# Performance work log

Measured on AMD Instinct MI355X. Metric: run time of the kernel, lower is better.

## Reference

```python
import jax, jax.numpy as jnp
import numpy as np

N_ATOMS = 200000
MAX_DEG = 6
DEG_COUNTS = [2000, 40000, 60000, 58000, 38000, 1500, 500]  # atoms of degree 0..6, sorted by degree
_OFF = np.concatenate([[0], np.cumsum(DEG_COUNTS)])
BATCH = 1024
N_TASKS = 12
NAF = 75
BN_SCALE = np.float32(1.0 / np.sqrt(1.0 + 1e-5))  # eval-mode BN, running stats (0, 1)


def _split(x):
    # static degree slicing (atoms sorted by degree)
    return [x[_OFF[d]:_OFF[d + 1]] for d in range(MAX_DEG + 1)]


def graph_conv(x, adjs, W, b):
    # W: [2*MAX_DEG+1, in, out]; per degree d>=1 weights (2(d-1): neighbors, 2d-1: self), last: degree-0 self
    sp = _split(x)
    outs = [None] * (MAX_DEG + 1)
    for d in range(1, MAX_DEG + 1):
        summed = x[adjs[d - 1]].sum(axis=1)  # [n_d, in] sum over d neighbors
        o = summed @ W[2 * (d - 1)] + b[2 * (d - 1)]
        o = o + sp[d] @ W[2 * d - 1] + b[2 * d - 1]
        outs[d] = o
    outs[0] = sp[0] @ W[2 * MAX_DEG] + b[2 * MAX_DEG]
    return jax.nn.relu(jnp.concatenate(outs, axis=0))


def graph_pool(x, adjs):
    # max over {self} U neighbors, per degree
    sp = _split(x)
    outs = [sp[0]]
    for d in range(1, MAX_DEG + 1):
        neigh = x[adjs[d - 1]]  # [n_d, d, nf]
        outs.append(jnp.concatenate([sp[d][:, None, :], neigh], axis=1).max(axis=1))
    return jnp.concatenate(outs, axis=0)


def bn(x, gamma, beta):
    return x * (gamma * BN_SCALE) + beta


def _forward(atom_features, conv0_W, conv0_b, conv1_W, conv1_b,
             bn0_gamma, bn0_beta, bn1_gamma, bn1_beta, bn2_gamma, bn2_beta,
             bn3_gamma, bn3_beta, dense0_W, dense0_b, dense1_W, dense1_b,
             reg_W, reg_b, unc_W, unc_b, membership, adjs, n_samples):
    x = graph_conv(atom_features, adjs, conv0_W, conv0_b)
    x = bn(x, bn0_gamma, bn0_beta)
    x = graph_pool(x, adjs)
    x = graph_conv(x, adjs, conv1_W, conv1_b)
    x = bn(x, bn1_gamma, bn1_beta)
    x = graph_pool(x, adjs)
    x = bn(jax.nn.relu(x @ dense0_W + dense0_b), bn2_gamma, bn2_beta)
    x = bn(jax.nn.relu(x @ dense1_W + dense1_b), bn3_gamma, bn3_beta)
    fp = jnp.tanh(jax.ops.segment_sum(x, membership, num_segments=BATCH))  # GraphGather
    out = (fp @ reg_W + reg_b)[:n_samples]
    log_var = (fp @ unc_W + unc_b)[:n_samples]
    var = jnp.exp(log_var)
    return (out, var, out, log_var, fp)


def setup_inputs():
    key = jax.random.key(0)
    ks = jax.random.split(key, 32)
    inp = {}
    inp['atom_features'] = jax.random.normal(ks[0], (N_ATOMS, NAF), jnp.float32)
    inp['degree_slice'] = jnp.stack([jnp.asarray(_OFF[:-1], jnp.int32), jnp.asarray(DEG_COUNTS, jnp.int32)], axis=1)
    inp['membership'] = jax.random.randint(ks[1], (N_ATOMS,), 0, BATCH, jnp.int32)
    inp['n_samples'] = BATCH
    for d in range(1, MAX_DEG + 1):
        inp['deg_adj_%d' % d] = jax.random.randint(ks[1 + d], (DEG_COUNTS[d], d), 0, N_ATOMS, jnp.int32)
    def w(k, shape):
        return jax.random.normal(k, shape, jnp.float32) * 0.05
    nW = 2 * MAX_DEG + 1
    inp['conv0_W'] = w(ks[8], (nW, NAF, 128)); inp['conv0_b'] = w(ks[9], (nW, 128))
    inp['conv1_W'] = w(ks[10], (nW, 128, 128)); inp['conv1_b'] = w(ks[11], (nW, 128))
    inp['bn0_gamma'] = 1.0 + w(ks[12], (128,)); inp['bn0_beta'] = w(ks[13], (128,))
    inp['bn1_gamma'] = 1.0 + w(ks[14], (128,)); inp['bn1_beta'] = w(ks[15], (128,))
    inp['bn2_gamma'] = 1.0 + w(ks[16], (64,)); inp['bn2_beta'] = w(ks[17], (64,))
    inp['bn3_gamma'] = 1.0 + w(ks[18], (64,)); inp['bn3_beta'] = w(ks[19], (64,))
    inp['dense0_W'] = w(ks[20], (128, 64)); inp['dense0_b'] = w(ks[21], (64,))
    inp['dense1_W'] = w(ks[22], (64, 64)); inp['dense1_b'] = w(ks[23], (64,))
    inp['reg_W'] = w(ks[24], (64, N_TASKS)); inp['reg_b'] = w(ks[25], (N_TASKS,))
    inp['unc_W'] = w(ks[26], (64, N_TASKS)); inp['unc_b'] = w(ks[27], (N_TASKS,))
    return inp


def reference(atom_features, conv0_W, conv0_b, conv1_W, conv1_b,
              bn0_gamma, bn0_beta, bn1_gamma, bn1_beta, bn2_gamma, bn2_beta,
              bn3_gamma, bn3_beta, dense0_W, dense0_b, dense1_W, dense1_b,
              reg_W, reg_b, unc_W, unc_b,
              degree_slice, membership, n_samples,
              deg_adj_1, deg_adj_2, deg_adj_3, deg_adj_4, deg_adj_5, deg_adj_6):
    adjs = [deg_adj_1, deg_adj_2, deg_adj_3, deg_adj_4, deg_adj_5, deg_adj_6]
    return _forward(atom_features, conv0_W, conv0_b, conv1_W, conv1_b,
                    bn0_gamma, bn0_beta, bn1_gamma, bn1_beta, bn2_gamma, bn2_beta,
                    bn3_gamma, bn3_beta, dense0_W, dense0_b, dense1_W, dense1_b,
                    reg_W, reg_b, unc_W, unc_b, membership, adjs, n_samples)
```

## Files before the change

### kernel.cpp

```cpp
#include <hip/hip_runtime.h>
#include <math.h>

constexpr int OFFS[8] = {0, 2000, 42000, 102000, 160000, 198000, 199500, 200000};
constexpr int CNT[7]  = {2000, 40000, 60000, 58000, 38000, 1500, 500};
constexpr int C_OFF[8] = {0, 32, 657, 1595, 2502, 3096, 3120, 3128};
constexpr int P_OFF[8] = {0, 250, 5250, 12750, 20000, 24750, 24938, 25001};
#define BN_SCALE_C 0.9999950000374997f

struct Adjs { const int* a[6]; };

typedef __attribute__((ext_vector_type(8))) short bf16x8;
typedef __attribute__((ext_vector_type(4))) float f32x4;

__device__ __forceinline__ void split1(float x, ushort& h, ushort& l) {
    const unsigned u = __float_as_uint(x);
    h = (ushort)(u >> 16);
    const float r = x - __uint_as_float(u & 0xffff0000u);
    l = (ushort)(__float_as_uint(r) >> 16);
}

__global__ __launch_bounds__(256)
void w1_convert_kernel(const float* __restrict__ W, ushort* __restrict__ hi,
                       ushort* __restrict__ lo) {
    const int t = blockIdx.x * 256 + threadIdx.x;
    if (t >= 13 * 8 * 4 * 64 * 8) return;
    const int i = t & 7, l = (t >> 3) & 63, ks = (t >> 9) & 3,
              g = (t >> 11) & 7, s = t >> 14;
    const int col = g * 16 + (l & 15);
    const int k = ks * 32 + (l >> 4) * 8 + i;
    ushort h, lw;
    split1(W[(size_t)(s * 128 + k) * 128 + col], h, lw);
    hi[t] = h; lo[t] = lw;
}

__global__ __launch_bounds__(256)
void w0_convert_kernel(const float* __restrict__ W, ushort* __restrict__ hi,
                       ushort* __restrict__ lo) {
    const int t = blockIdx.x * 256 + threadIdx.x;
    if (t >= 7 * 8 * 5 * 64 * 8) return;
    const int i = t & 7;
    const int r = t >> 3;
    const int l = r & 63;
    const int r2 = r >> 6;
    const int ks = r2 % 5;
    const int r3 = r2 / 5;
    const int g = r3 & 7, d = r3 >> 3;
    const int col = g * 16 + (l & 15);
    const int k = ks * 32 + (l >> 4) * 8 + i;
    float v = 0.f;
    if (d == 0) {
        if (k < 75) v = W[(size_t)(12 * 75 + k) * 128 + col];
    } else {
        if (k < 75)       v = W[(size_t)((2 * d - 2) * 75 + k) * 128 + col];
        else if (k < 150) v = W[(size_t)((2 * d - 1) * 75 + (k - 75)) * 128 + col];
    }
    ushort h, lw;
    split1(v, h, lw);
    hi[t] = h; lo[t] = lw;
}

template<int KSTEPS, int SROW>
__device__ __forceinline__ void mfma_gemm(const ushort* sa_hi, const ushort* sa_lo,
                                          const ushort* wp_hi, const ushort* wp_lo,
                                          f32x4 acc[8], int l, int w)
{
    const int lr = l & 15, lq = l >> 4;
    const size_t lb = (size_t)l * 8;
    #pragma unroll
    for (int ks = 0; ks < KSTEPS; ++ks) {
        const int kb = ks * 32 + lq * 8;
        const bf16x8 ah = *(const bf16x8*)(sa_hi + (size_t)(w * 16 + lr) * SROW + kb);
        const bf16x8 al = *(const bf16x8*)(sa_lo + (size_t)(w * 16 + lr) * SROW + kb);
        bf16x8 bh0 = *(const bf16x8*)(wp_hi + (size_t)(0 * KSTEPS + ks) * 512 + lb);
        bf16x8 bl0 = *(const bf16x8*)(wp_lo + (size_t)(0 * KSTEPS + ks) * 512 + lb);
        bf16x8 bh1 = *(const bf16x8*)(wp_hi + (size_t)(1 * KSTEPS + ks) * 512 + lb);
        bf16x8 bl1 = *(const bf16x8*)(wp_lo + (size_t)(1 * KSTEPS + ks) * 512 + lb);
        #pragma unroll
        for (int g = 0; g < 8; ++g) {
            bf16x8 bh2 = bh0, bl2 = bl0;
            if (g < 6) {
                bh2 = *(const bf16x8*)(wp_hi + (size_t)((g + 2) * KSTEPS + ks) * 512 + lb);
                bl2 = *(const bf16x8*)(wp_lo + (size_t)((g + 2) * KSTEPS + ks) * 512 + lb);
            }
            acc[g] = __builtin_amdgcn_mfma_f32_16x16x32_bf16(ah, bh0, acc[g], 0, 0, 0);
            acc[g] = __builtin_amdgcn_mfma_f32_16x16x32_bf16(al, bh0, acc[g], 0, 0, 0);
            acc[g] = __builtin_amdgcn_mfma_f32_16x16x32_bf16(ah, bl0, acc[g], 0, 0, 0);
            bh0 = bh1; bl0 = bl1; bh1 = bh2; bl1 = bl2;
        }
    }
}

__device__ __forceinline__ void mfma_epilogue(f32x4 acc[8], float* fs,
                                              const float* s_eb, float* out,
                                              int a0, int nat, int tid)
{
    const int l = tid & 63, w = tid >> 6, lr = l & 15, lq = l >> 4;
    __syncthreads();
    #pragma unroll
    for (int g = 0; g < 8; ++g)
        #pragma unroll
        for (int r = 0; r < 4; ++r)
            fs[(size_t)(w * 16 + lq * 4 + r) * 132 + g * 16 + lr] = acc[g][r];
    __syncthreads();
    #pragma unroll
    for (int p = 0; p < 8; ++p) {
        const int row = p * 8 + (tid >> 5);
        if (row < nat) {
            const int c = (tid & 31) * 4;
            const float4 v  = *(const float4*)&fs[(size_t)row * 132 + c];
            const float4 bb = *(const float4*)&s_eb[c];
            const float4 gs = *(const float4*)&s_eb[128 + c];
            const float4 be = *(const float4*)&s_eb[256 + c];
            float4 o;
            o.x = fmaxf(v.x + bb.x, 0.f) * gs.x + be.x;
            o.y = fmaxf(v.y + bb.y, 0.f) * gs.y + be.y;
            o.z = fmaxf(v.z + bb.z, 0.f) * gs.z + be.z;
            o.w = fmaxf(v.w + bb.w, 0.f) * gs.w + be.w;
            *(float4*)(out + (size_t)(a0 + row) * 128 + c) = o;
        }
    }
}

template<int D>
__device__ __forceinline__ void conv0_body(int tile, const float* __restrict__ x,
    const ushort* __restrict__ wp_hi, const ushort* __restrict__ wp_lo,
    const float* __restrict__ b, const float* __restrict__ gamma,
    const float* __restrict__ beta, const int* __restrict__ adjp,
    float* __restrict__ out, ushort* s_ahi, ushort* s_alo, int* s_adj,
    float* s_eb, int tid)
{
    constexpr int SROW = 168;
    const int a0 = OFFS[D] + tile * 64;
    const int nat = min(64, OFFS[D + 1] - a0);

    if (tid < 128) {
        float bb;
        if constexpr (D > 0)
            bb = b[(2 * D - 2) * 128 + tid] + b[(2 * D - 1) * 128 + tid];
        else
            bb = b[12 * 128 + tid];
        s_eb[tid] = bb;
        s_eb[128 + tid] = gamma[tid] * BN_SCALE_C;
        s_eb[256 + tid] = beta[tid];
    }
    if constexpr (D > 0) {
        for (int e = tid; e < 64 * D; e += 256) {
            const int al = e / D;
            if (al < nat)
                s_adj[e] = adjp[(size_t)(a0 - OFFS[D] + al) * D + (e - al * D)];
        }
        __syncthreads();
    }
    if constexpr (D == 0) {
        for (int e = tid; e < 64 * 85; e += 256) {
            const int al = e / 85, k = 75 + e - (e / 85) * 85;
            s_ahi[al * SROW + k] = 0; s_alo[al * SROW + k] = 0;
        }
    } else {
        for (int e = tid; e < 64 * 10; e += 256) {
            const int al = e / 10, k = 150 + e - (e / 10) * 10;
            s_ahi[al * SROW + k] = 0; s_alo[al * SROW + k] = 0;
        }
    }
    #pragma unroll 4
    for (int p = 0; p < 19; ++p) {
        const int e = p * 256 + tid;
        if (e < 4800) {
            const int al = e / 75;
            const int kk = e - al * 75;
            if (al < nat) {
                const float self = x[(size_t)(a0 + al) * 75 + kk];
                ushort h, l;
                if constexpr (D > 0) {
                    float sum = 0.f;
                    #pragma unroll
                    for (int i = 0; i < D; ++i)
                        sum += x[(size_t)s_adj[al * D + i] * 75 + kk];
                    split1(sum, h, l);
                    s_ahi[al * SROW + kk] = h; s_alo[al * SROW + kk] = l;
                    split1(self, h, l);
                    s_ahi[al * SROW + 75 + kk] = h; s_alo[al * SROW + 75 + kk] = l;
                } else {
                    split1(self, h, l);
                    s_ahi[al * SROW + kk] = h; s_alo[al * SROW + kk] = l;
                }
            }
        }
    }
    __syncthreads();

    const int l = tid & 63, w = tid >> 6;
    f32x4 acc[8];
    #pragma unroll
    for (int g = 0; g < 8; ++g) acc[g] = (f32x4){0.f, 0.f, 0.f, 0.f};
    mfma_gemm<5, SROW>(s_ahi, s_alo, wp_hi + (size_t)D * 20480,
                       wp_lo + (size_t)D * 20480, acc, l, w);
    mfma_epilogue(acc, (float*)s_ahi, s_eb, out, a0, nat, tid);
}

__global__ __launch_bounds__(256, 3)
void conv0_merged(const float* __restrict__ x, const ushort* __restrict__ wp_hi,
                  const ushort* __restrict__ wp_lo, const float* __restrict__ b,
                  const float* __restrict__ gamma, const float* __restrict__ beta,
                  Adjs adj, float* __restrict__ out)
{
    __shared__ ushort s_a[2][64 * 168];
    __shared__ int s_adj[64 * 6];
    __shared__ float s_eb[384];
    const int blk = blockIdx.x, tid = threadIdx.x;
    #define C0(D) conv0_body<D>(blk - C_OFF[D], x, wp_hi, wp_lo, b, gamma, beta, \
        (D > 0) ? adj.a[D - 1] : nullptr, out, s_a[0], s_a[1], s_adj, s_eb, tid)
    if      (blk < C_OFF[1]) C0(0);
    else if (blk < C_OFF[2]) C0(1);
    else if (blk < C_OFF[3]) C0(2);
    else if (blk < C_OFF[4]) C0(3);
    else if (blk < C_OFF[5]) C0(4);
    else if (blk < C_OFF[6]) C0(5);
    else                     C0(6);
    #undef C0
}

template<int D, bool PHASE0>
__device__ __forceinline__ void conv1_stage(const float* __restrict__ x,
    ushort* s_ahi, ushort* s_alo, const int* s_adj, int a0, int nat, int tid)
{
    constexpr int SROW = 136;
    #pragma unroll 2
    for (int p = 0; p < 8; ++p) {
        const int e = p * 256 + tid;
        const int al = e >> 5, c = e & 31;
        if (al < nat) {
            float4 v;
            if (PHASE0 && D > 0) {
                v = make_float4(0.f, 0.f, 0.f, 0.f);
                #pragma unroll
                for (int i = 0; i < D; ++i) {
                    const float4 t = *((const float4*)(x + (size_t)s_adj[al * D + i] * 128) + c);
                    v.x += t.x; v.y += t.y; v.z += t.z; v.w += t.w;
                }
            } else {
                v = *((const float4*)(x + (size_t)(a0 + al) * 128) + c);
            }
            ushort4 h, lo;
            split1(v.x, h.x, lo.x); split1(v.y, h.y, lo.y);
            split1(v.z, h.z, lo.z); split1(v.w, h.w, lo.w);
            *(ushort4*)&s_ahi[al * SROW + c * 4] = h;
            *(ushort4*)&s_alo[al * SROW + c * 4] = lo;
        }
    }
}

template<int D>
__device__ __forceinline__ void conv1_body(int tile, const float* __restrict__ x,
    const ushort* __restrict__ wp_hi, const ushort* __restrict__ wp_lo,
    const float* __restrict__ b, const float* __restrict__ gamma,
    const float* __restrict__ beta, const int* __restrict__ adjp,
    float* __restrict__ out, ushort* s_ahi, ushort* s_alo, int* s_adj,
    float* s_eb, int tid)
{
    constexpr int SROW = 136;
    const int a0 = OFFS[D] + tile * 64;
    const int nat = min(64, OFFS[D + 1] - a0);

    if (tid < 128) {
        float bb;
        if constexpr (D > 0)
            bb = b[(2 * D - 2) * 128 + tid] + b[(2 * D - 1) * 128 + tid];
        else
            bb = b[12 * 128 + tid];
        s_eb[tid] = bb;
        s_eb[128 + tid] = gamma[tid] * BN_SCALE_C;
        s_eb[256 + tid] = beta[tid];
    }
    if constexpr (D > 0) {
        for (int e = tid; e < 64 * D; e += 256) {
            const int al = e / D;
            if (al < nat)
                s_adj[e] = adjp[(size_t)(a0 - OFFS[D] + al) * D + (e - al * D)];
        }
        __syncthreads();
    }

    const int l = tid & 63, w = tid >> 6;
    f32x4 acc[8];
    #pragma unroll
    for (int g = 0; g < 8; ++g) acc[g] = (f32x4){0.f, 0.f, 0.f, 0.f};

    conv1_stage<D, true>(x, s_ahi, s_alo, s_adj, a0, nat, tid);
    __syncthreads();
    {
        const size_t wb = (size_t)((D == 0) ? 12 : (2 * D - 2)) * 16384;
        mfma_gemm<4, SROW>(s_ahi, s_alo, wp_hi + wb, wp_lo + wb, acc, l, w);
    }
    if constexpr (D > 0) {
        __syncthreads();
        conv1_stage<D, false>(x, s_ahi, s_alo, s_adj, a0, nat, tid);
        __syncthreads();
        const size_t wb = (size_t)(2 * D - 1) * 16384;
        mfma_gemm<4, SROW>(s_ahi, s_alo, wp_hi + wb, wp_lo + wb, acc, l, w);
    }
    mfma_epilogue(acc, (float*)s_ahi, s_eb, out, a0, nat, tid);
}

__global__ __launch_bounds__(256, 4)
void conv1_merged(const float* __restrict__ x, const ushort* __restrict__ wp_hi,
                  const ushort* __restrict__ wp_lo, const float* __restrict__ b,
                  const float* __restrict__ gamma, const float* __restrict__ beta,
                  Adjs adj, float* __restrict__ out)
{
    __shared__ ushort s_a[2][64 * 136];
    __shared__ int s_adj[64 * 6];
    __shared__ float s_eb[384];
    const int blk = blockIdx.x, tid = threadIdx.x;
    #define C1(D) conv1_body<D>(blk - C_OFF[D], x, wp_hi, wp_lo, b, gamma, beta, \
        (D > 0) ? adj.a[D - 1] : nullptr, out, s_a[0], s_a[1], s_adj, s_eb, tid)
    if      (blk < C_OFF[1]) C1(0);
    else if (blk < C_OFF[2]) C1(1);
    else if (blk < C_OFF[3]) C1(2);
    else if (blk < C_OFF[4]) C1(3);
    else if (blk < C_OFF[5]) C1(4);
    else if (blk < C_OFF[6]) C1(5);
    else                     C1(6);
    #undef C1
}

template<int D>
__device__ __forceinline__ void pool_body(int tile, const float* __restrict__ x,
    const int* __restrict__ adjp, float* __restrict__ out, int tid)
{
    const int tx = tid & 31;
    const int ai = tile * 8 + (tid >> 5);
    if (ai >= CNT[D]) return;
    const int a = OFFS[D] + ai;
    float4 v = *((const float4*)(x + (size_t)a * 128) + tx);
    if constexpr (D > 0) {
        #pragma unroll
        for (int i = 0; i < D; ++i) {
            const int n = adjp[(size_t)ai * D + i];
            const float4 t = *((const float4*)(x + (size_t)n * 128) + tx);
            v.x = fmaxf(v.x, t.x); v.y = fmaxf(v.y, t.y);
            v.z = fmaxf(v.z, t.z); v.w = fmaxf(v.w, t.w);
        }
    }
    *((float4*)(out + (size_t)a * 128) + tx) = v;
}

__global__ __launch_bounds__(256)
void pool_merged(const float* __restrict__ x, Adjs adj, float* __restrict__ out)
{
    const int blk = blockIdx.x, tid = threadIdx.x;
    #define PB(D) pool_body<D>(blk - P_OFF[D], x, (D > 0) ? adj.a[D - 1] : nullptr, out, tid)
    if      (blk < P_OFF[1]) PB(0);
    else if (blk < P_OFF[2]) PB(1);
    else if (blk < P_OFF[3]) PB(2);
    else if (blk < P_OFF[4]) PB(3);
    else if (blk < P_OFF[5]) PB(4);
    else if (blk < P_OFF[6]) PB(5);
    else                     PB(6);
    #undef PB
}

template<int D>
__device__ __forceinline__ void d0_body(int tile, const float* __restrict__ x,
    const float* __restrict__ W, const float* __restrict__ b,
    const float* __restrict__ gamma, const float* __restrict__ beta,
    const int* __restrict__ adjp, float* __restrict__ out,
    float* s_a , int* s_adj, int tid)
{
    const int a0 = OFFS[D] + tile * 64;
    const int nat = min(64, OFFS[D + 1] - a0);

    if constexpr (D > 0) {
        for (int e = tid; e < 64 * D; e += 256) {
            const int al = e / D;
            if (al < nat)
                s_adj[e] = adjp[(size_t)(a0 - OFFS[D] + al) * D + (e - al * D)];
        }
        __syncthreads();
    }
    {
        const int tx4 = tid & 31, ag = tid >> 5;
        #pragma unroll
        for (int ap = 0; ap < 8; ++ap) {
            const int al = ap * 8 + ag;
            if (al < nat) {
                float4 v = *((const float4*)(x + (size_t)(a0 + al) * 128) + tx4);
                if constexpr (D > 0) {
                    #pragma unroll
                    for (int i = 0; i < D; ++i) {
                        const float4 t =
                            *((const float4*)(x + (size_t)s_adj[al * D + i] * 128) + tx4);
                        v.x = fmaxf(v.x, t.x); v.y = fmaxf(v.y, t.y);
                        v.z = fmaxf(v.z, t.z); v.w = fmaxf(v.w, t.w);
                    }
                }
                *(float4*)&s_a[al * 132 + tx4 * 4] = v;
            }
        }
    }
    __syncthreads();

    const int tx = tid & 15, ty = tid >> 4;
    float acc[4][4];
    #pragma unroll
    for (int i = 0; i < 4; ++i)
        #pragma unroll
        for (int j = 0; j < 4; ++j) acc[i][j] = 0.f;

    #pragma unroll 4
    for (int k4 = 0; k4 < 32; ++k4) {
        float4 wk[4];
        #pragma unroll
        for (int kk = 0; kk < 4; ++kk)
            wk[kk] = *(const float4*)(W + (size_t)(k4 * 4 + kk) * 64 + tx * 4);
        #pragma unroll
        for (int i = 0; i < 4; ++i) {
            const float4 av = *(const float4*)&s_a[(ty * 4 + i) * 132 + k4 * 4];
            acc[i][0] = fmaf(av.x, wk[0].x, acc[i][0]);
            acc[i][1] = fmaf(av.x, wk[0].y, acc[i][1]);
            acc[i][2] = fmaf(av.x, wk[0].z, acc[i][2]);
            acc[i][3] = fmaf(av.x, wk[0].w, acc[i][3]);
            acc[i][0] = fmaf(av.y, wk[1].x, acc[i][0]);
            acc[i][1] = fmaf(av.y, wk[1].y, acc[i][1]);
            acc[i][2] = fmaf(av.y, wk[1].z, acc[i][2]);
            acc[i][3] = fmaf(av.y, wk[1].w, acc[i][3]);
            acc[i][0] = fmaf(av.z, wk[2].x, acc[i][0]);
            acc[i][1] = fmaf(av.z, wk[2].y, acc[i][1]);
            acc[i][2] = fmaf(av.z, wk[2].z, acc[i][2]);
            acc[i][3] = fmaf(av.z, wk[2].w, acc[i][3]);
            acc[i][0] = fmaf(av.w, wk[3].x, acc[i][0]);
            acc[i][1] = fmaf(av.w, wk[3].y, acc[i][1]);
            acc[i][2] = fmaf(av.w, wk[3].z, acc[i][2]);
            acc[i][3] = fmaf(av.w, wk[3].w, acc[i][3]);
        }
    }
    const int j = tx * 4;
    float bb[4], gs[4], be[4];
    #pragma unroll
    for (int c = 0; c < 4; ++c) {
        bb[c] = b[j + c]; gs[c] = gamma[j + c] * BN_SCALE_C; be[c] = beta[j + c];
    }
    #pragma unroll
    for (int i = 0; i < 4; ++i) {
        const int al = ty * 4 + i;
        if (al < nat) {
            float4 o;
            o.x = fmaxf(acc[i][0] + bb[0], 0.f) * gs[0] + be[0];
            o.y = fmaxf(acc[i][1] + bb[1], 0.f) * gs[1] + be[1];
            o.z = fmaxf(acc[i][2] + bb[2], 0.f) * gs[2] + be[2];
            o.w = fmaxf(acc[i][3] + bb[3], 0.f) * gs[3] + be[3];
            *(float4*)(out + (size_t)(a0 + al) * 64 + j) = o;
        }
    }
}

__global__ __launch_bounds__(256, 4)
void dense0_pool_merged(const float* __restrict__ x, const float* __restrict__ W,
                        const float* __restrict__ b, const float* __restrict__ gamma,
                        const float* __restrict__ beta, Adjs adj,
                        float* __restrict__ out)
{
    __shared__ float s_a[64 * 132];
    __shared__ int s_adj[64 * 6];
    const int blk = blockIdx.x, tid = threadIdx.x;
    #define D0(D) d0_body<D>(blk - C_OFF[D], x, W, b, gamma, beta, \
        (D > 0) ? adj.a[D - 1] : nullptr, out, s_a, s_adj, tid)
    if      (blk < C_OFF[1]) D0(0);
    else if (blk < C_OFF[2]) D0(1);
    else if (blk < C_OFF[3]) D0(2);
    else if (blk < C_OFF[4]) D0(3);
    else if (blk < C_OFF[5]) D0(4);
    else if (blk < C_OFF[6]) D0(5);
    else                     D0(6);
    #undef D0
}

__global__ void zero_counts_kernel(int* __restrict__ counts) {
    counts[blockIdx.x * 256 + threadIdx.x] = 0;
}

__global__ __launch_bounds__(256)
void hist_kernel(const int* __restrict__ mem, int* __restrict__ counts) {
    const int a = blockIdx.x * 256 + threadIdx.x;
    if (a < 200000) atomicAdd(&counts[mem[a]], 1);
}

__global__ __launch_bounds__(1024)
void scan_kernel(const int* __restrict__ counts, int* __restrict__ starts,
                 int* __restrict__ cursor) {
    __shared__ int s[1024];
    const int tid = threadIdx.x;
    s[tid] = counts[tid];
    __syncthreads();
    #pragma unroll
    for (int off = 1; off < 1024; off <<= 1) {
        const int v = (tid >= off) ? s[tid - off] : 0;
        __syncthreads();
        s[tid] += v;
        __syncthreads();
    }
    const int st = (tid == 0) ? 0 : s[tid - 1];
    starts[tid] = st;
    cursor[tid] = st;
    if (tid == 1023) starts[1024] = s[1023];
}

__global__ __launch_bounds__(256)
void scatter_kernel(const int* __restrict__ mem, int* __restrict__ cursor,
                    int* __restrict__ idx) {
    const int a = blockIdx.x * 256 + threadIdx.x;
    if (a < 200000) {
        const int p = atomicAdd(&cursor[mem[a]], 1);
        idx[p] = a;
    }
}

__global__ __launch_bounds__(256, 4)
void seg_dense1_kernel(const float* __restrict__ y0, const float* __restrict__ W,
                       const float* __restrict__ b, const float* __restrict__ gamma,
                       const float* __restrict__ beta, const int* __restrict__ idx,
                       const int* __restrict__ starts, float* __restrict__ accum)
{
    __shared__ float s_a[64][68];
    __shared__ float s_w[64][64];
    __shared__ float s_red[16][64];
    const int tid = threadIdx.x;
    const int seg = blockIdx.x;
    const int s0 = starts[seg];
    const int cnt = starts[seg + 1] - s0;

    #pragma unroll
    for (int p = 0; p < 4; ++p) {
        const int f = p * 256 + tid;
        const int r = f >> 4, c = (f & 15) * 4;
        *(float4*)&s_w[r][c] = *(const float4*)(W + r * 64 + c);
    }

    const int tx = tid & 15, ty = tid >> 4;
    const int j = tx * 4;
    float bb[4], gs[4], be[4];
    #pragma unroll
    for (int c = 0; c < 4; ++c) {
        bb[c] = b[j + c]; gs[c] = gamma[j + c] * BN_SCALE_C; be[c] = beta[j + c];
    }
    float facc[4] = {0.f, 0.f, 0.f, 0.f};

    for (int t0 = 0; t0 < cnt; t0 += 64) {
        const int nt = min(64, cnt - t0);
        __syncthreads();
        #pragma unroll
        for (int p = 0; p < 4; ++p) {
            const int e = p * 256 + tid;
            const int al = e >> 4, c = e & 15;
            if (al < nt) {
                const int a = idx[s0 + t0 + al];
                *(float4*)&s_a[al][c * 4] = *((const float4*)(y0 + (size_t)a * 64) + c);
            }
        }
        __syncthreads();
        float acc[4][4];
        #pragma unroll
        for (int i = 0; i < 4; ++i)
            #pragma unroll
            for (int c = 0; c < 4; ++c) acc[i][c] = 0.f;
        #pragma unroll 8
        for (int k = 0; k < 64; ++k) {
            const float4 w = *(float4*)&s_w[k][tx * 4];
            #pragma unroll
            for (int i = 0; i < 4; ++i) {
                const float av = s_a[ty * 4 + i][k];
                acc[i][0] = fmaf(av, w.x, acc[i][0]);
                acc[i][1] = fmaf(av, w.y, acc[i][1]);
                acc[i][2] = fmaf(av, w.z, acc[i][2]);
                acc[i][3] = fmaf(av, w.w, acc[i][3]);
            }
        }
        #pragma unroll
        for (int i = 0; i < 4; ++i) {
            if (ty * 4 + i < nt) {
                #pragma unroll
                for (int c = 0; c < 4; ++c)
                    facc[c] += fmaxf(acc[i][c] + bb[c], 0.f) * gs[c] + be[c];
            }
        }
    }
    __syncthreads();
    #pragma unroll
    for (int c = 0; c < 4; ++c) s_red[ty][j + c] = facc[c];
    __syncthreads();
    if (tid < 64) {
        float s = 0.f;
        #pragma unroll
        for (int q = 0; q < 16; ++q) s += s_red[q][tid];
        accum[(size_t)seg * 64 + tid] = s;
    }
}

__global__ __launch_bounds__(256)
void final_kernel(const float* __restrict__ accum,
                  const float* __restrict__ regW, const float* __restrict__ regb,
                  const float* __restrict__ uncW, const float* __restrict__ uncb,
                  float* __restrict__ out)
{
    __shared__ float s_f[256];
    const int tid = threadIdx.x;
    const int rl = tid >> 6;
    const int c = tid & 63;
    const int r = blockIdx.x * 4 + rl;
    const float f = tanhf(accum[(size_t)r * 64 + c]);
    out[49152 + (size_t)r * 64 + c] = f;
    s_f[tid] = f;
    __syncthreads();
    if (c < 24) {
        const bool isreg = (c < 12);
        const int t = isreg ? c : c - 12;
        const float* Wm = isreg ? regW : uncW;
        float a = isreg ? regb[t] : uncb[t];
        #pragma unroll 8
        for (int k = 0; k < 64; ++k)
            a = fmaf(s_f[rl * 64 + k], Wm[k * 12 + t], a);
        if (isreg) {
            out[(size_t)r * 12 + t] = a;
            out[24576 + (size_t)r * 12 + t] = a;
        } else {
            out[36864 + (size_t)r * 12 + t] = a;
            out[12288 + (size_t)r * 12 + t] = expf(a);
        }
    }
}

extern "C" void kernel_launch(void* const* d_in, const int* in_sizes, int n_in,
                              void* d_out, int out_size, void* d_ws, size_t ws_size,
                              hipStream_t stream)
{
    const float* atom_features = (const float*)d_in[0];
    const int*   membership    = (const int*)d_in[2];
    Adjs adj;
    for (int d = 1; d <= 6; ++d) adj.a[d - 1] = (const int*)d_in[3 + d];
    const float* conv0_W = (const float*)d_in[10];
    const float* conv0_b = (const float*)d_in[11];
    const float* conv1_W = (const float*)d_in[12];
    const float* conv1_b = (const float*)d_in[13];
    const float* bn0_g = (const float*)d_in[14];
    const float* bn0_b = (const float*)d_in[15];
    const float* bn1_g = (const float*)d_in[16];
    const float* bn1_b = (const float*)d_in[17];
    const float* bn2_g = (const float*)d_in[18];
    const float* bn2_b = (const float*)d_in[19];
    const float* bn3_g = (const float*)d_in[20];
    const float* bn3_b = (const float*)d_in[21];
    const float* dense0_W = (const float*)d_in[22];
    const float* dense0_b = (const float*)d_in[23];
    const float* dense1_W = (const float*)d_in[24];
    const float* dense1_b = (const float*)d_in[25];
    const float* reg_W = (const float*)d_in[26];
    const float* reg_b = (const float*)d_in[27];
    const float* unc_W = (const float*)d_in[28];
    const float* unc_b = (const float*)d_in[29];

    float* ws    = (float*)d_ws;
    float* buf0  = ws;
    float* buf1  = ws + 25600000;
    float* accum = ws + 51200000;
    int*   idx     = (int*)(ws + 51265536);
    int*   counts  = (int*)(ws + 51465536);
    int*   starts  = (int*)(ws + 51466560);
    int*   cursor  = (int*)(ws + 51467585);
    ushort* wp1_hi = (ushort*)(ws + 51468800);
    ushort* wp1_lo = (ushort*)(ws + 51575296);
    ushort* wp0_hi = (ushort*)(ws + 51681792);
    ushort* wp0_lo = (ushort*)(ws + 51753472);

    w1_convert_kernel<<<832, 256, 0, stream>>>(conv1_W, wp1_hi, wp1_lo);
    w0_convert_kernel<<<560, 256, 0, stream>>>(conv0_W, wp0_hi, wp0_lo);
    zero_counts_kernel<<<4, 256, 0, stream>>>(counts);
    hist_kernel<<<782, 256, 0, stream>>>(membership, counts);
    scan_kernel<<<1, 1024, 0, stream>>>(counts, starts, cursor);
    scatter_kernel<<<782, 256, 0, stream>>>(membership, cursor, idx);

    conv0_merged<<<3128, 256, 0, stream>>>(atom_features, wp0_hi, wp0_lo, conv0_b,
                                           bn0_g, bn0_b, adj, buf0);
    pool_merged<<<25001, 256, 0, stream>>>(buf0, adj, buf1);
    conv1_merged<<<3128, 256, 0, stream>>>(buf1, wp1_hi, wp1_lo, conv1_b,
                                           bn1_g, bn1_b, adj, buf0);
    dense0_pool_merged<<<3128, 256, 0, stream>>>(buf0, dense0_W, dense0_b,
                                                 bn2_g, bn2_b, adj, buf1);
    seg_dense1_kernel<<<1024, 256, 0, stream>>>(buf1, dense1_W, dense1_b,
                                                bn3_g, bn3_b, idx, starts, accum);
    final_kernel<<<256, 256, 0, stream>>>(accum, reg_W, reg_b, unc_W, unc_b, (float*)d_out);
}
```

Before: 533.7 us.

## Gather conv operands straight into MFMA registers, dropping LDS staging

Both graph-conv kernels now have each lane gather and sum its own neighbor rows directly into registers, split them into bf16 hi/lo fragments, and feed the MFMAs without staging the A tiles through shared memory. Conv0's weight packing is changed to per-matrix 3 k-steps instead of fused 5-step concatenated neighbor/self blocks. The epilogue is reduced to a 32-row shared buffer processed in two halves, which cuts LDS use and allows higher occupancy for conv0. The cost is redundant, less coalesced global loads, since each lane reads 8 contiguous floats of a row, and an extra k-step of zero padding for conv0's self part.

```diff
diff --git a/kernel.cpp b/kernel.cpp
--- a/kernel.cpp
+++ b/kernel.cpp
@@ -17,6 +17,15 @@
     h = (ushort)(u >> 16);
     const float r = x - __uint_as_float(u & 0xffff0000u);
     l = (ushort)(__float_as_uint(r) >> 16);
+}
+
+__device__ __forceinline__ void split8a(const float s[8], bf16x8& hv, bf16x8& lv) {
+    #pragma unroll
+    for (int i = 0; i < 8; ++i) {
+        ushort h, lo;
+        split1(s[i], h, lo);
+        hv[i] = (short)h; lv[i] = (short)lo;
+    }
 }
 
 __global__ __launch_bounds__(256)
@@ -37,179 +46,176 @@
 void w0_convert_kernel(const float* __restrict__ W, ushort* __restrict__ hi,
                        ushort* __restrict__ lo) {
     const int t = blockIdx.x * 256 + threadIdx.x;
-    if (t >= 7 * 8 * 5 * 64 * 8) return;
+    if (t >= 13 * 8 * 3 * 64 * 8) return;
     const int i = t & 7;
-    const int r = t >> 3;
-    const int l = r & 63;
-    const int r2 = r >> 6;
-    const int ks = r2 % 5;
-    const int r3 = r2 / 5;
-    const int g = r3 & 7, d = r3 >> 3;
+    const int l = (t >> 3) & 63;
+    const int r2 = t >> 9;
+    const int ks = r2 % 3;
+    const int r3 = r2 / 3;
+    const int g = r3 & 7, m = r3 >> 3;
     const int col = g * 16 + (l & 15);
     const int k = ks * 32 + (l >> 4) * 8 + i;
     float v = 0.f;
-    if (d == 0) {
-        if (k < 75) v = W[(size_t)(12 * 75 + k) * 128 + col];
-    } else {
-        if (k < 75)       v = W[(size_t)((2 * d - 2) * 75 + k) * 128 + col];
-        else if (k < 150) v = W[(size_t)((2 * d - 1) * 75 + (k - 75)) * 128 + col];
-    }
+    if (k < 75) v = W[(size_t)(m * 75 + k) * 128 + col];
     ushort h, lw;
     split1(v, h, lw);
     hi[t] = h; lo[t] = lw;
 }
 
-template<int KSTEPS, int SROW>
-__device__ __forceinline__ void mfma_gemm(const ushort* sa_hi, const ushort* sa_lo,
-                                          const ushort* wp_hi, const ushort* wp_lo,
-                                          f32x4 acc[8], int l, int w)
-{
-    const int lr = l & 15, lq = l >> 4;
-    const size_t lb = (size_t)l * 8;
-    #pragma unroll
-    for (int ks = 0; ks < KSTEPS; ++ks) {
-        const int kb = ks * 32 + lq * 8;
-        const bf16x8 ah = *(const bf16x8*)(sa_hi + (size_t)(w * 16 + lr) * SROW + kb);
-        const bf16x8 al = *(const bf16x8*)(sa_lo + (size_t)(w * 16 + lr) * SROW + kb);
-        bf16x8 bh0 = *(const bf16x8*)(wp_hi + (size_t)(0 * KSTEPS + ks) * 512 + lb);
-        bf16x8 bl0 = *(const bf16x8*)(wp_lo + (size_t)(0 * KSTEPS + ks) * 512 + lb);
-        bf16x8 bh1 = *(const bf16x8*)(wp_hi + (size_t)(1 * KSTEPS + ks) * 512 + lb);
-        bf16x8 bl1 = *(const bf16x8*)(wp_lo + (size_t)(1 * KSTEPS + ks) * 512 + lb);
-        #pragma unroll
-        for (int g = 0; g < 8; ++g) {
-            bf16x8 bh2 = bh0, bl2 = bl0;
-            if (g < 6) {
-                bh2 = *(const bf16x8*)(wp_hi + (size_t)((g + 2) * KSTEPS + ks) * 512 + lb);
-                bl2 = *(const bf16x8*)(wp_lo + (size_t)((g + 2) * KSTEPS + ks) * 512 + lb);
-            }
-            acc[g] = __builtin_amdgcn_mfma_f32_16x16x32_bf16(ah, bh0, acc[g], 0, 0, 0);
-            acc[g] = __builtin_amdgcn_mfma_f32_16x16x32_bf16(al, bh0, acc[g], 0, 0, 0);
-            acc[g] = __builtin_amdgcn_mfma_f32_16x16x32_bf16(ah, bl0, acc[g], 0, 0, 0);
-            bh0 = bh1; bl0 = bl1; bh1 = bh2; bl1 = bl2;
-        }
-    }
-}
-
-__device__ __forceinline__ void mfma_epilogue(f32x4 acc[8], float* fs,
-                                              const float* s_eb, float* out,
-                                              int a0, int nat, int tid)
-{
-    const int l = tid & 63, w = tid >> 6, lr = l & 15, lq = l >> 4;
-    __syncthreads();
-    #pragma unroll
-    for (int g = 0; g < 8; ++g)
-        #pragma unroll
-        for (int r = 0; r < 4; ++r)
-            fs[(size_t)(w * 16 + lq * 4 + r) * 132 + g * 16 + lr] = acc[g][r];
-    __syncthreads();
-    #pragma unroll
-    for (int p = 0; p < 8; ++p) {
-        const int row = p * 8 + (tid >> 5);
-        if (row < nat) {
-            const int c = (tid & 31) * 4;
-            const float4 v  = *(const float4*)&fs[(size_t)row * 132 + c];
-            const float4 bb = *(const float4*)&s_eb[c];
-            const float4 gs = *(const float4*)&s_eb[128 + c];
-            const float4 be = *(const float4*)&s_eb[256 + c];
-            float4 o;
-            o.x = fmaxf(v.x + bb.x, 0.f) * gs.x + be.x;
-            o.y = fmaxf(v.y + bb.y, 0.f) * gs.y + be.y;
-            o.z = fmaxf(v.z + bb.z, 0.f) * gs.z + be.z;
-            o.w = fmaxf(v.w + bb.w, 0.f) * gs.w + be.w;
-            *(float4*)(out + (size_t)(a0 + row) * 128 + c) = o;
-        }
-    }
-}
-
-template<int D>
-__device__ __forceinline__ void conv0_body(int tile, const float* __restrict__ x,
+template<int ROWLEN>
+__device__ __forceinline__ void row_acc(const float* __restrict__ row, int k0,
+                                        float s[8]) {
+    if constexpr (ROWLEN == 128) {
+        const float4 a = *(const float4*)(row + k0);
+        const float4 b = *(const float4*)(row + k0 + 4);
+        s[0] += a.x; s[1] += a.y; s[2] += a.z; s[3] += a.w;
+        s[4] += b.x; s[5] += b.y; s[6] += b.z; s[7] += b.w;
+    } else {
+        #pragma unroll
+        for (int i = 0; i < 8; ++i)
+            if (k0 + i < ROWLEN) s[i] += row[k0 + i];
+    }
+}
+
+template<int KS>
+__device__ __forceinline__ void gemm_ks(const ushort* __restrict__ wh,
+                                        const ushort* __restrict__ wl,
+                                        int ks, size_t lb,
+                                        bf16x8 ah, bf16x8 al_, f32x4 acc[8])
+{
+    bf16x8 bh0 = *(const bf16x8*)(wh + (size_t)(0 * KS + ks) * 512 + lb);
+    bf16x8 bl0 = *(const bf16x8*)(wl + (size_t)(0 * KS + ks) * 512 + lb);
+    bf16x8 bh1 = *(const bf16x8*)(wh + (size_t)(1 * KS + ks) * 512 + lb);
+    bf16x8 bl1 = *(const bf16x8*)(wl + (size_t)(1 * KS + ks) * 512 + lb);
+    #pragma unroll
+    for (int g = 0; g < 8; ++g) {
+        bf16x8 bh2 = bh0, bl2 = bl0;
+        if (g < 6) {
+            bh2 = *(const bf16x8*)(wh + (size_t)((g + 2) * KS + ks) * 512 + lb);
+            bl2 = *(const bf16x8*)(wl + (size_t)((g + 2) * KS + ks) * 512 + lb);
+        }
+        acc[g] = __builtin_amdgcn_mfma_f32_16x16x32_bf16(ah, bh0, acc[g], 0, 0, 0);
+        acc[g] = __builtin_amdgcn_mfma_f32_16x16x32_bf16(al_, bh0, acc[g], 0, 0, 0);
+        acc[g] = __builtin_amdgcn_mfma_f32_16x16x32_bf16(ah, bl0, acc[g], 0, 0, 0);
+        bh0 = bh1; bl0 = bl1; bh1 = bh2; bl1 = bl2;
+    }
+}
+
+template<int D, int ROWLEN, int KS>
+__device__ __forceinline__ void conv_body(int tile, const float* __restrict__ x,
     const ushort* __restrict__ wp_hi, const ushort* __restrict__ wp_lo,
-    const float* __restrict__ b, const float* __restrict__ gamma,
+    const float* __restrict__ bias, const float* __restrict__ gamma,
     const float* __restrict__ beta, const int* __restrict__ adjp,
-    float* __restrict__ out, ushort* s_ahi, ushort* s_alo, int* s_adj,
-    float* s_eb, int tid)
-{
-    constexpr int SROW = 168;
+    float* __restrict__ out, float* fs, float* s_eb, int tid)
+{
     const int a0 = OFFS[D] + tile * 64;
     const int nat = min(64, OFFS[D + 1] - a0);
+    const int l = tid & 63, w = tid >> 6, lr = l & 15, lq = l >> 4;
 
     if (tid < 128) {
         float bb;
         if constexpr (D > 0)
-            bb = b[(2 * D - 2) * 128 + tid] + b[(2 * D - 1) * 128 + tid];
+            bb = bias[(2 * D - 2) * 128 + tid] + bias[(2 * D - 1) * 128 + tid];
         else
-            bb = b[12 * 128 + tid];
+            bb = bias[12 * 128 + tid];
         s_eb[tid] = bb;
         s_eb[128 + tid] = gamma[tid] * BN_SCALE_C;
         s_eb[256 + tid] = beta[tid];
     }
+
+    const int rowa = min(a0 + w * 16 + lr, OFFS[D + 1] - 1);
+    int nb[(D > 0) ? D : 1];
     if constexpr (D > 0) {
-        for (int e = tid; e < 64 * D; e += 256) {
-            const int al = e / D;
-            if (al < nat)
-                s_adj[e] = adjp[(size_t)(a0 - OFFS[D] + al) * D + (e - al * D)];
+        #pragma unroll
+        for (int j = 0; j < D; ++j)
+            nb[j] = adjp[(size_t)(rowa - OFFS[D]) * D + j];
+    }
+
+    f32x4 acc[8];
+    #pragma unroll
+    for (int g = 0; g < 8; ++g) acc[g] = (f32x4){0.f, 0.f, 0.f, 0.f};
+
+    const size_t lb = (size_t)l * 8;
+
+    {
+        const int m = (D == 0) ? 12 : (2 * D - 2);
+        const ushort* wh = wp_hi + (size_t)m * (8 * KS * 512);
+        const ushort* wl = wp_lo + (size_t)m * (8 * KS * 512);
+        #pragma unroll
+        for (int ks = 0; ks < KS; ++ks) {
+            const int k0 = ks * 32 + lq * 8;
+            float s[8] = {0.f, 0.f, 0.f, 0.f, 0.f, 0.f, 0.f, 0.f};
+            if constexpr (D > 0) {
+                #pragma unroll
+                for (int j = 0; j < D; ++j)
+                    row_acc<ROWLEN>(x + (size_t)nb[j] * ROWLEN, k0, s);
+            } else {
+                row_acc<ROWLEN>(x + (size_t)rowa * ROWLEN, k0, s);
+            }
+            bf16x8 ah, al_;
+            split8a(s, ah, al_);
+            gemm_ks<KS>(wh, wl, ks, lb, ah, al_, acc);
+        }
+    }
+    if constexpr (D > 0) {
+        const ushort* wh = wp_hi + (size_t)(2 * D - 1) * (8 * KS * 512);
+        const ushort* wl = wp_lo + (size_t)(2 * D - 1) * (8 * KS * 512);
+        #pragma unroll
+        for (int ks = 0; ks < KS; ++ks) {
+            const int k0 = ks * 32 + lq * 8;
+            float s[8] = {0.f, 0.f, 0.f, 0.f, 0.f, 0.f, 0.f, 0.f};
+            row_acc<ROWLEN>(x + (size_t)rowa * ROWLEN, k0, s);
+            bf16x8 ah, al_;
+            split8a(s, ah, al_);
+            gemm_ks<KS>(wh, wl, ks, lb, ah, al_, acc);
+        }
+    }
+
+    __syncthreads();
+    #pragma unroll
+    for (int h = 0; h < 2; ++h) {
+        if ((w >> 1) == h) {
+            const int wloc = w & 1;
+            #pragma unroll
+            for (int g = 0; g < 8; ++g)
+                #pragma unroll
+                for (int r = 0; r < 4; ++r)
+                    fs[(wloc * 16 + lq * 4 + r) * 132 + g * 16 + lr] = acc[g][r];
         }
         __syncthreads();
-    }
-    if constexpr (D == 0) {
-        for (int e = tid; e < 64 * 85; e += 256) {
-            const int al = e / 85, k = 75 + e - (e / 85) * 85;
-            s_ahi[al * SROW + k] = 0; s_alo[al * SROW + k] = 0;
-        }
-    } else {
-        for (int e = tid; e < 64 * 10; e += 256) {
-            const int al = e / 10, k = 150 + e - (e / 10) * 10;
-            s_ahi[al * SROW + k] = 0; s_alo[al * SROW + k] = 0;
-        }
-    }
-    #pragma unroll 4
-    for (int p = 0; p < 19; ++p) {
-        const int e = p * 256 + tid;
-        if (e < 4800) {
-            const int al = e / 75;
-            const int kk = e - al * 75;
-            if (al < nat) {
-                const float self = x[(size_t)(a0 + al) * 75 + kk];
-                ushort h, l;
-                if constexpr (D > 0) {
-                    float sum = 0.f;
-                    #pragma unroll
-                    for (int i = 0; i < D; ++i)
-                        sum += x[(size_t)s_adj[al * D + i] * 75 + kk];
-                    split1(sum, h, l);
-                    s_ahi[al * SROW + kk] = h; s_alo[al * SROW + kk] = l;
-                    split1(self, h, l);
-                    s_ahi[al * SROW + 75 + kk] = h; s_alo[al * SROW + 75 + kk] = l;
-                } else {
-                    split1(self, h, l);
-                    s_ahi[al * SROW + kk] = h; s_alo[al * SROW + kk] = l;
-                }
+        #pragma unroll
+        for (int p = 0; p < 4; ++p) {
+            const int fr = p * 8 + (tid >> 5);
+            const int row = h * 32 + fr;
+            if (row < nat) {
+                const int c = (tid & 31) * 4;
+                const float4 v  = *(const float4*)&fs[fr * 132 + c];
+                const float4 bb = *(const float4*)&s_eb[c];
+                const float4 gs = *(const float4*)&s_eb[128 + c];
+                const float4 be = *(const float4*)&s_eb[256 + c];
+                float4 o;
+                o.x = fmaxf(v.x + bb.x, 0.f) * gs.x + be.x;
+                o.y = fmaxf(v.y + bb.y, 0.f) * gs.y + be.y;
+                o.z = fmaxf(v.z + bb.z, 0.f) * gs.z + be.z;
+                o.w = fmaxf(v.w + bb.w, 0.f) * gs.w + be.w;
+                *(float4*)(out + (size_t)(a0 + row) * 128 + c) = o;
             }
         }
-    }
-    __syncthreads();
-
-    const int l = tid & 63, w = tid >> 6;
-    f32x4 acc[8];
-    #pragma unroll
-    for (int g = 0; g < 8; ++g) acc[g] = (f32x4){0.f, 0.f, 0.f, 0.f};
-    mfma_gemm<5, SROW>(s_ahi, s_alo, wp_hi + (size_t)D * 20480,
-                       wp_lo + (size_t)D * 20480, acc, l, w);
-    mfma_epilogue(acc, (float*)s_ahi, s_eb, out, a0, nat, tid);
-}
-
-__global__ __launch_bounds__(256, 3)
+        __syncthreads();
+    }
+}
+
+__global__ __launch_bounds__(256, 4)
 void conv0_merged(const float* __restrict__ x, const ushort* __restrict__ wp_hi,
                   const ushort* __restrict__ wp_lo, const float* __restrict__ b,
                   const float* __restrict__ gamma, const float* __restrict__ beta,
                   Adjs adj, float* __restrict__ out)
 {
-    __shared__ ushort s_a[2][64 * 168];
-    __shared__ int s_adj[64 * 6];
+    __shared__ float fs[32 * 132];
     __shared__ float s_eb[384];
     const int blk = blockIdx.x, tid = threadIdx.x;
-    #define C0(D) conv0_body<D>(blk - C_OFF[D], x, wp_hi, wp_lo, b, gamma, beta, \
-        (D > 0) ? adj.a[D - 1] : nullptr, out, s_a[0], s_a[1], s_adj, s_eb, tid)
+    #define C0(D) conv_body<D, 75, 3>(blk - C_OFF[D], x, wp_hi, wp_lo, b, gamma, \
+        beta, (D > 0) ? adj.a[D - 1] : nullptr, out, fs, s_eb, tid)
     if      (blk < C_OFF[1]) C0(0);
     else if (blk < C_OFF[2]) C0(1);
     else if (blk < C_OFF[3]) C0(2);
@@ -220,100 +226,17 @@
     #undef C0
 }
 
-template<int D, bool PHASE0>
-__device__ __forceinline__ void conv1_stage(const float* __restrict__ x,
-    ushort* s_ahi, ushort* s_alo, const int* s_adj, int a0, int nat, int tid)
-{
-    constexpr int SROW = 136;
-    #pragma unroll 2
-    for (int p = 0; p < 8; ++p) {
-        const int e = p * 256 + tid;
-        const int al = e >> 5, c = e & 31;
-        if (al < nat) {
-            float4 v;
-            if (PHASE0 && D > 0) {
-                v = make_float4(0.f, 0.f, 0.f, 0.f);
-                #pragma unroll
-                for (int i = 0; i < D; ++i) {
-                    const float4 t = *((const float4*)(x + (size_t)s_adj[al * D + i] * 128) + c);
-                    v.x += t.x; v.y += t.y; v.z += t.z; v.w += t.w;
-                }
-            } else {
-                v = *((const float4*)(x + (size_t)(a0 + al) * 128) + c);
-            }
-            ushort4 h, lo;
-            split1(v.x, h.x, lo.x); split1(v.y, h.y, lo.y);
-            split1(v.z, h.z, lo.z); split1(v.w, h.w, lo.w);
-            *(ushort4*)&s_ahi[al * SROW + c * 4] = h;
-            *(ushort4*)&s_alo[al * SROW + c * 4] = lo;
-        }
-    }
-}
-
-template<int D>
-__device__ __forceinline__ void conv1_body(int tile, const float* __restrict__ x,
-    const ushort* __restrict__ wp_hi, const ushort* __restrict__ wp_lo,
-    const float* __restrict__ b, const float* __restrict__ gamma,
-    const float* __restrict__ beta, const int* __restrict__ adjp,
-    float* __restrict__ out, ushort* s_ahi, ushort* s_alo, int* s_adj,
-    float* s_eb, int tid)
-{
-    constexpr int SROW = 136;
-    const int a0 = OFFS[D] + tile * 64;
-    const int nat = min(64, OFFS[D + 1] - a0);
-
-    if (tid < 128) {
-        float bb;
-        if constexpr (D > 0)
-            bb = b[(2 * D - 2) * 128 + tid] + b[(2 * D - 1) * 128 + tid];
-        else
-            bb = b[12 * 128 + tid];
-        s_eb[tid] = bb;
-        s_eb[128 + tid] = gamma[tid] * BN_SCALE_C;
-        s_eb[256 + tid] = beta[tid];
-    }
-    if constexpr (D > 0) {
-        for (int e = tid; e < 64 * D; e += 256) {
-            const int al = e / D;
-            if (al < nat)
-                s_adj[e] = adjp[(size_t)(a0 - OFFS[D] + al) * D + (e - al * D)];
-        }
-        __syncthreads();
-    }
-
-    const int l = tid & 63, w = tid >> 6;
-    f32x4 acc[8];
-    #pragma unroll
-    for (int g = 0; g < 8; ++g) acc[g] = (f32x4){0.f, 0.f, 0.f, 0.f};
-
-    conv1_stage<D, true>(x, s_ahi, s_alo, s_adj, a0, nat, tid);
-    __syncthreads();
-    {
-        const size_t wb = (size_t)((D == 0) ? 12 : (2 * D - 2)) * 16384;
-        mfma_gemm<4, SROW>(s_ahi, s_alo, wp_hi + wb, wp_lo + wb, acc, l, w);
-    }
-    if constexpr (D > 0) {
-        __syncthreads();
-        conv1_stage<D, false>(x, s_ahi, s_alo, s_adj, a0, nat, tid);
-        __syncthreads();
-        const size_t wb = (size_t)(2 * D - 1) * 16384;
-        mfma_gemm<4, SROW>(s_ahi, s_alo, wp_hi + wb, wp_lo + wb, acc, l, w);
-    }
-    mfma_epilogue(acc, (float*)s_ahi, s_eb, out, a0, nat, tid);
-}
-
 __global__ __launch_bounds__(256, 4)
 void conv1_merged(const float* __restrict__ x, const ushort* __restrict__ wp_hi,
                   const ushort* __restrict__ wp_lo, const float* __restrict__ b,
                   const float* __restrict__ gamma, const float* __restrict__ beta,
                   Adjs adj, float* __restrict__ out)
 {
-    __shared__ ushort s_a[2][64 * 136];
-    __shared__ int s_adj[64 * 6];
+    __shared__ float fs[32 * 132];
     __shared__ float s_eb[384];
     const int blk = blockIdx.x, tid = threadIdx.x;
-    #define C1(D) conv1_body<D>(blk - C_OFF[D], x, wp_hi, wp_lo, b, gamma, beta, \
-        (D > 0) ? adj.a[D - 1] : nullptr, out, s_a[0], s_a[1], s_adj, s_eb, tid)
+    #define C1(D) conv_body<D, 128, 4>(blk - C_OFF[D], x, wp_hi, wp_lo, b, gamma, \
+        beta, (D > 0) ? adj.a[D - 1] : nullptr, out, fs, s_eb, tid)
     if      (blk < C_OFF[1]) C1(0);
     else if (blk < C_OFF[2]) C1(1);
     else if (blk < C_OFF[3]) C1(2);
@@ -669,10 +592,10 @@
     ushort* wp1_hi = (ushort*)(ws + 51468800);
     ushort* wp1_lo = (ushort*)(ws + 51575296);
     ushort* wp0_hi = (ushort*)(ws + 51681792);
-    ushort* wp0_lo = (ushort*)(ws + 51753472);
+    ushort* wp0_lo = (ushort*)(ws + 51761664);
 
     w1_convert_kernel<<<832, 256, 0, stream>>>(conv1_W, wp1_hi, wp1_lo);
-    w0_convert_kernel<<<560, 256, 0, stream>>>(conv0_W, wp0_hi, wp0_lo);
+    w0_convert_kernel<<<624, 256, 0, stream>>>(conv0_W, wp0_hi, wp0_lo);
     zero_counts_kernel<<<4, 256, 0, stream>>>(counts);
     hist_kernel<<<782, 256, 0, stream>>>(membership, counts);
     scan_kernel<<<1, 1024, 0, stream>>>(counts, starts, cursor);
```

Result: no change. 538.3 us (+0.9%).
